# Optimization experiments

Measured on AMD Instinct MI355X. Metric: run time of the kernel, lower is better.

## Reference

```python
import jax, jax.numpy as jnp
import numpy as np

B, S, D_IN, D_OUT = 4, 2048, 1024, 1024


def setup_inputs() -> dict:
    key = jax.random.key(0)
    ks = jax.random.split(key, 7)
    s_in = 1.0 / np.sqrt(D_IN)
    return {
        "x": jax.random.normal(ks[0], (B, S, D_IN), dtype=jnp.float32),
        "Wq": jax.random.uniform(ks[1], (D_IN, D_OUT), jnp.float32, -s_in, s_in),
        "bq": jax.random.uniform(ks[2], (D_OUT,), jnp.float32, -s_in, s_in),
        "Wk": jax.random.uniform(ks[3], (D_IN, D_OUT), jnp.float32, -s_in, s_in),
        "bk": jax.random.uniform(ks[4], (D_OUT,), jnp.float32, -s_in, s_in),
        "Wv": jax.random.uniform(ks[5], (D_IN, D_OUT), jnp.float32, -s_in, s_in),
        "bv": jax.random.uniform(ks[6], (D_OUT,), jnp.float32, -s_in, s_in),
    }


def reference(x, Wq, bq, Wk, bk, Wv, bv):
    # q,k,v: [B, S, D_OUT]
    q = jnp.einsum("bsd,de->bse", x, Wq) + bq
    k = jnp.einsum("bsd,de->bse", x, Wk) + bk
    v = jnp.einsum("bsd,de->bse", x, Wv) + bv
    scale = 1.0 / jnp.sqrt(jnp.asarray(q.shape[-1], q.dtype))
    scores = jnp.einsum("bqe,bke->bqk", q, k) * scale  # [B, S, S]
    attn = jax.nn.softmax(scores, axis=-1)
    return jnp.einsum("bqk,bke->bqe", attn, v)
```

## Files before the change

### kernel.cpp

```cpp
#include <hip/hip_runtime.h>
#include <hip/hip_bf16.h>
#include <stdint.h>


#define Bsz 4
#define Ssz 2048
#define Dsz 1024

typedef __attribute__((ext_vector_type(8))) short short8;
typedef __attribute__((ext_vector_type(4))) float floatx4;
typedef const __attribute__((address_space(1))) void* gptr_t;
typedef __attribute__((address_space(3))) void* lptr_t;

__device__ __forceinline__ ushort f32_to_bf16(float f) {
    union { float f; uint32_t u; } c; c.f = f;
    uint32_t u = c.u;
    u += 0x7fffu + ((u >> 16) & 1u);
    return (ushort)(u >> 16);
}

__device__ __forceinline__ void glds16(const ushort* g, ushort* l) {
    __builtin_amdgcn_global_load_lds((gptr_t)g, (lptr_t)l, 16, 0, 0);
}

__device__ __forceinline__ void barrier_raw() {
    asm volatile("" ::: "memory");
    __builtin_amdgcn_s_barrier();
    asm volatile("" ::: "memory");
}

#define MFMA_QUAD(MB, NB)                                                              \
    _Pragma("unroll")                                                                  \
    for (int m_ = 0; m_ < 4; m_++) {                                                   \
        _Pragma("unroll")                                                              \
        for (int n_ = 0; n_ < 2; n_++) {                                               \
            acc[(MB) * 4 + m_][(NB) * 2 + n_] = __builtin_amdgcn_mfma_f32_16x16x32_bf16( \
                af[m_][0], bf[(NB) * 2 + n_][0], acc[(MB) * 4 + m_][(NB) * 2 + n_], 0, 0, 0); \
            acc[(MB) * 4 + m_][(NB) * 2 + n_] = __builtin_amdgcn_mfma_f32_16x16x32_bf16( \
                af[m_][1], bf[(NB) * 2 + n_][1], acc[(MB) * 4 + m_][(NB) * 2 + n_], 0, 0, 0); \
        }                                                                              \
    }

#define LOAD_A(half)                                                                   \
    _Pragma("unroll")                                                                  \
    for (int m_ = 0; m_ < 4; m_++) {                                                   \
        af[m_][0] = *(const short8*)(lA + aBase + ((half) * 4 + m_) * 1024 + c0);      \
        af[m_][1] = *(const short8*)(lA + aBase + ((half) * 4 + m_) * 1024 + c1);      \
    }

#define LOAD_B(pn)                                                                     \
    _Pragma("unroll")                                                                  \
    for (int n_ = 0; n_ < 2; n_++) {                                                   \
        bf[(pn) * 2 + n_][0] = *(const short8*)(lB + bBase + ((pn) * 2 + n_) * 1024 + c0); \
        bf[(pn) * 2 + n_][1] = *(const short8*)(lB + bBase + ((pn) * 2 + n_) * 1024 + c1); \
    }

template <int NT>
__device__ __forceinline__ void gemm256_core(
    const ushort* __restrict__ A, int lda,
    const ushort* __restrict__ Bt, int ldb,
    int row0, int col0, floatx4 (&acc)[8][4])
{
    __shared__ __align__(16) ushort lsA[2][256 * 64];
    __shared__ __align__(16) ushort lsB[2][256 * 64];

    const int tid  = threadIdx.x;
    const int lane = tid & 63;
    const int wave = tid >> 6;
    const int wr   = (wave >> 2) * 128;
    const int wc   = (wave & 3) * 64;
    const int m16  = lane & 15;
    const int quad = lane >> 4;

#pragma unroll
    for (int i = 0; i < 8; i++)
#pragma unroll
        for (int j = 0; j < 4; j++) acc[i][j] = (floatx4){0.f, 0.f, 0.f, 0.f};

    const int sRow = tid >> 3;
    const int sC   = ((tid & 7) ^ (sRow & 7)) * 8;
    const ushort* aSrc = A  + (size_t)(row0 + sRow) * lda + sC;
    const ushort* bSrc = Bt + (size_t)(col0 + sRow) * ldb + sC;
    ushort* dA = &lsA[0][0] + tid * 8;
    ushort* dB = &lsB[0][0] + tid * 8;

    const int aBase = (wr + m16) * 64;
    const int bBase = (wc + m16) * 64;
    const int c0 = (quad ^ (m16 & 7)) * 8;
    const int c1 = c0 ^ 32;

    auto stage = [&](int kt, int buf, int pair) {
        const size_t ko = (size_t)kt * 64;
        const int bo = buf * 16384;
        if (pair == 0) {
            glds16(aSrc + ko,                      dA + bo);
            glds16(aSrc + ko + (size_t)64 * lda,   dA + bo + 4096);
        } else if (pair == 1) {
            glds16(aSrc + ko + (size_t)128 * lda,  dA + bo + 8192);
            glds16(aSrc + ko + (size_t)192 * lda,  dA + bo + 12288);
        } else if (pair == 2) {
            glds16(bSrc + ko,                      dB + bo);
            glds16(bSrc + ko + (size_t)64 * ldb,   dB + bo + 4096);
        } else {
            glds16(bSrc + ko + (size_t)128 * ldb,  dB + bo + 8192);
            glds16(bSrc + ko + (size_t)192 * ldb,  dB + bo + 12288);
        }
    };

    stage(0, 0, 0); stage(0, 0, 1); stage(0, 0, 2); stage(0, 0, 3);
    stage(1, 1, 0);
    asm volatile("s_waitcnt vmcnt(2)" ::: "memory");
    barrier_raw();

    short8 af[4][2], bf[4][2];

    for (int kt = 0; kt < NT; ++kt) {
        const int buf = kt & 1;
        const ushort* lA = &lsA[buf][0];
        const ushort* lB = &lsB[buf][0];
        const bool pf1 = (kt + 1 < NT);

        LOAD_A(0);
        LOAD_B(0);
        if (pf1) stage(kt + 1, buf ^ 1, 1);
        barrier_raw();
        __builtin_amdgcn_s_setprio(1);
        MFMA_QUAD(0, 0);
        __builtin_amdgcn_s_setprio(0);
        barrier_raw();

        LOAD_B(1);
        if (pf1) stage(kt + 1, buf ^ 1, 2);
        barrier_raw();
        __builtin_amdgcn_s_setprio(1);
        MFMA_QUAD(0, 1);
        __builtin_amdgcn_s_setprio(0);
        barrier_raw();

        LOAD_A(1);
        if (pf1) stage(kt + 1, buf ^ 1, 3);
        barrier_raw();
        __builtin_amdgcn_s_setprio(1);
        MFMA_QUAD(1, 0);
        __builtin_amdgcn_s_setprio(0);
        barrier_raw();

        if (kt + 2 < NT) stage(kt + 2, buf, 0);
        __builtin_amdgcn_s_setprio(1);
        MFMA_QUAD(1, 1);
        __builtin_amdgcn_s_setprio(0);
        if (kt + 2 < NT)      { asm volatile("s_waitcnt vmcnt(2)" ::: "memory"); }
        else if (kt + 1 < NT) { asm volatile("s_waitcnt vmcnt(0)" ::: "memory"); }
        barrier_raw();
    }
}

__global__ __launch_bounds__(512, 2) void k_qkv256(
    const ushort* __restrict__ xb, const ushort* __restrict__ Wt,
    const float* __restrict__ bq, const float* __restrict__ bk,
    const float* __restrict__ bv, ushort* __restrict__ QKV,
    ushort* __restrict__ Vt)
{
    const int bid = blockIdx.x;
    const int wg  = (bid & 7) * 48 + (bid >> 3);
    const int bm  = wg & 31;
    const int bn  = wg >> 5;
    const int row0  = bm * 256;
    const int col0n = bn * 256;

    floatx4 acc[8][4];
    gemm256_core<16>(xb, Dsz, Wt, Dsz, row0, col0n, acc);

    const int tid  = threadIdx.x;
    const int lane = tid & 63;
    const int wave = tid >> 6;
    const int wr   = (wave >> 2) * 128;
    const int wc   = (wave & 3) * 64;
    const int m16  = lane & 15;
    const int quad = lane >> 4;

    const int z     = bn >> 2;
    const int colz0 = col0n & 1023;

    if (z == 0) {
#pragma unroll
        for (int ni = 0; ni < 4; ni++) {
            const int colz = colz0 + wc + ni * 16 + m16;
            const float bqv = bq[colz];
#pragma unroll
            for (int mi = 0; mi < 8; mi++) {
                const int grow0 = row0 + wr + mi * 16 + quad * 4;
#pragma unroll
                for (int j = 0; j < 4; j++)
                    QKV[(size_t)(grow0 + j) * Dsz + colz] =
                        f32_to_bf16((acc[mi][ni][j] + bqv) * 0.03125f);
            }
        }
    } else if (z == 1) {
        ushort* Kout = QKV + (size_t)(Bsz * Ssz) * Dsz;
#pragma unroll
        for (int ni = 0; ni < 4; ni++) {
            const int colz = colz0 + wc + ni * 16 + m16;
            const float bkv = bk[colz];
#pragma unroll
            for (int mi = 0; mi < 8; mi++) {
                const int grow0 = row0 + wr + mi * 16 + quad * 4;
#pragma unroll
                for (int j = 0; j < 4; j++)
                    Kout[(size_t)(grow0 + j) * Dsz + colz] =
                        f32_to_bf16(acc[mi][ni][j] + bkv);
            }
        }
    } else {
#pragma unroll
        for (int ni = 0; ni < 4; ni++) {
            const int colz = colz0 + wc + ni * 16 + m16;
            const float bvv = bv[colz];
#pragma unroll
            for (int mi = 0; mi < 8; mi++) {
                const int grow0 = row0 + wr + mi * 16 + quad * 4;
                ushort4 vpack;
                vpack.x = f32_to_bf16(acc[mi][ni][0] + bvv);
                vpack.y = f32_to_bf16(acc[mi][ni][1] + bvv);
                vpack.z = f32_to_bf16(acc[mi][ni][2] + bvv);
                vpack.w = f32_to_bf16(acc[mi][ni][3] + bvv);
                const int batch = grow0 >> 11;
                const int s0 = grow0 & (Ssz - 1);
                *(ushort4*)&Vt[(size_t)batch * Dsz * Ssz + (size_t)colz * Ssz + s0] = vpack;
            }
        }
    }
}

__global__ __launch_bounds__(512, 2) void k_scores256(
    const ushort* __restrict__ QKV, float* __restrict__ scores)
{
    const int bid = blockIdx.x;
    const int wg  = (bid & 7) * 32 + (bid >> 3);
    const int b   = wg >> 6;
    const int bm  = (wg >> 3) & 7;
    const int bn  = wg & 7;
    const int row0 = bm * 256;
    const int col0 = bn * 256;

    const ushort* Q  = QKV + (size_t)b * Ssz * Dsz;
    const ushort* Kb = QKV + (size_t)(Bsz + b) * Ssz * Dsz;

    floatx4 acc[8][4];
    gemm256_core<16>(Q, Dsz, Kb, Dsz, row0, col0, acc);

    const int tid  = threadIdx.x;
    const int lane = tid & 63;
    const int wave = tid >> 6;
    const int wr   = (wave >> 2) * 128;
    const int wc   = (wave & 3) * 64;
    const int m16  = lane & 15;
    const int quad = lane >> 4;

    float* out = scores + (size_t)b * Ssz * Ssz;
#pragma unroll
    for (int ni = 0; ni < 4; ni++) {
        const int gcol = col0 + wc + ni * 16 + m16;
#pragma unroll
        for (int mi = 0; mi < 8; mi++) {
            const int grow0 = row0 + wr + mi * 16 + quad * 4;
#pragma unroll
            for (int j = 0; j < 4; j++)
                out[(size_t)(grow0 + j) * Ssz + gcol] = acc[mi][ni][j];
        }
    }
}

template <bool OUT_BF16>
__device__ __forceinline__ void gemm128(
    int bx, int by,
    const ushort* __restrict__ A, int lda,
    const ushort* __restrict__ Bt, int ldb,
    int K,
    void* __restrict__ Cout, int ldc,
    const float* __restrict__ bias, float alpha)
{
    __shared__ ushort lsA[2][128 * 32];
    __shared__ ushort lsB[2][128 * 32];

    const int tid  = threadIdx.x;
    const int row0 = by * 128;
    const int col0 = bx * 128;

    const int lane = tid & 63;
    const int wave = tid >> 6;
    const int wr   = (wave >> 1) * 64;
    const int wc   = (wave & 1) * 64;
    const int m16  = lane & 15;
    const int quad = lane >> 4;

    floatx4 acc[4][4];
#pragma unroll
    for (int i = 0; i < 4; i++)
#pragma unroll
        for (int j = 0; j < 4; j++) acc[i][j] = (floatx4){0.f, 0.f, 0.f, 0.f};

    const int srow = tid >> 2;
    const int skc  = (tid & 3) ^ ((srow >> 1) & 3);
    const ushort* ga = A  + (size_t)(row0 + srow) * lda + skc * 8;
    const ushort* gb = Bt + (size_t)(col0 + srow) * ldb + skc * 8;
    const int aoff = (quad ^ ((m16 >> 1) & 3)) * 8;

    __builtin_amdgcn_global_load_lds((gptr_t)(ga),                     (lptr_t)(lsA[0] + tid * 8),        16, 0, 0);
    __builtin_amdgcn_global_load_lds((gptr_t)(ga + (size_t)64 * lda), (lptr_t)(lsA[0] + 2048 + tid * 8), 16, 0, 0);
    __builtin_amdgcn_global_load_lds((gptr_t)(gb),                     (lptr_t)(lsB[0] + tid * 8),        16, 0, 0);
    __builtin_amdgcn_global_load_lds((gptr_t)(gb + (size_t)64 * ldb), (lptr_t)(lsB[0] + 2048 + tid * 8), 16, 0, 0);

    for (int k0 = 0; k0 < K; k0 += 32) {
        const int cur = (k0 >> 5) & 1;
        __syncthreads();
        if (k0 + 32 < K) {
            const int nxt = cur ^ 1;
            const int kn = k0 + 32;
            __builtin_amdgcn_global_load_lds((gptr_t)(ga + kn),                     (lptr_t)(lsA[nxt] + tid * 8),        16, 0, 0);
            __builtin_amdgcn_global_load_lds((gptr_t)(ga + kn + (size_t)64 * lda), (lptr_t)(lsA[nxt] + 2048 + tid * 8), 16, 0, 0);
            __builtin_amdgcn_global_load_lds((gptr_t)(gb + kn),                     (lptr_t)(lsB[nxt] + tid * 8),        16, 0, 0);
            __builtin_amdgcn_global_load_lds((gptr_t)(gb + kn + (size_t)64 * ldb), (lptr_t)(lsB[nxt] + 2048 + tid * 8), 16, 0, 0);
        }

        short8 af[4], bfr[4];
#pragma unroll
        for (int mi = 0; mi < 4; mi++)
            af[mi] = *(const short8*)&lsA[cur][(wr + mi * 16 + m16) * 32 + aoff];
#pragma unroll
        for (int ni = 0; ni < 4; ni++)
            bfr[ni] = *(const short8*)&lsB[cur][(wc + ni * 16 + m16) * 32 + aoff];
#pragma unroll
        for (int mi = 0; mi < 4; mi++)
#pragma unroll
            for (int ni = 0; ni < 4; ni++)
                acc[mi][ni] = __builtin_amdgcn_mfma_f32_16x16x32_bf16(af[mi], bfr[ni], acc[mi][ni], 0, 0, 0);
    }

#pragma unroll
    for (int ni = 0; ni < 4; ni++) {
        const int gcol = col0 + wc + ni * 16 + m16;
        const float bv = bias ? bias[gcol] : 0.0f;
#pragma unroll
        for (int mi = 0; mi < 4; mi++) {
            const int grow0 = row0 + wr + mi * 16 + quad * 4;
#pragma unroll
            for (int j = 0; j < 4; j++) {
                float v = (acc[mi][ni][j] + bv) * alpha;
                if (OUT_BF16)
                    ((ushort*)Cout)[(size_t)(grow0 + j) * ldc + gcol] = f32_to_bf16(v);
                else
                    ((float*)Cout)[(size_t)(grow0 + j) * ldc + gcol] = v;
            }
        }
    }
}

__global__ __launch_bounds__(256) void k_cvt_x(const float* __restrict__ x, ushort* __restrict__ xb) {
    int i = (blockIdx.x * 256 + threadIdx.x) * 4;
    float4 v = *(const float4*)(x + i);
    ushort4 o;
    o.x = f32_to_bf16(v.x); o.y = f32_to_bf16(v.y);
    o.z = f32_to_bf16(v.z); o.w = f32_to_bf16(v.w);
    *(ushort4*)(xb + i) = o;
}

__global__ __launch_bounds__(256) void k_wt(const float* __restrict__ Wq, const float* __restrict__ Wk,
                                            const float* __restrict__ Wv, ushort* __restrict__ Wt) {
    __shared__ float tile[32][33];
    const int z = blockIdx.z;
    const float* W = (z == 0) ? Wq : ((z == 1) ? Wk : Wv);
    ushort* out = Wt + (size_t)z * Dsz * Dsz;
    const int kb = blockIdx.y * 32, nb = blockIdx.x * 32;
    const int tx = threadIdx.x, ty = threadIdx.y;
#pragma unroll
    for (int j = 0; j < 32; j += 8)
        tile[ty + j][tx] = W[(size_t)(kb + ty + j) * Dsz + nb + tx];
    __syncthreads();
#pragma unroll
    for (int j = 0; j < 32; j += 8)
        out[(size_t)(nb + ty + j) * Dsz + kb + tx] = f32_to_bf16(tile[tx][ty + j]);
}

__global__ __launch_bounds__(256) void k_softmax(float* __restrict__ scores) {
    const size_t row = blockIdx.x;
    float* rp = scores + row * Ssz;
    const int tid = threadIdx.x;
    float4 v0 = ((const float4*)rp)[tid];
    float4 v1 = ((const float4*)rp)[tid + 256];
    float m = fmaxf(fmaxf(fmaxf(v0.x, v0.y), fmaxf(v0.z, v0.w)),
                    fmaxf(fmaxf(v1.x, v1.y), fmaxf(v1.z, v1.w)));
#pragma unroll
    for (int o = 32; o > 0; o >>= 1) m = fmaxf(m, __shfl_down(m, o, 64));
    __shared__ float redm[4];
    if ((tid & 63) == 0) redm[tid >> 6] = m;
    __syncthreads();
    const float rm = fmaxf(fmaxf(redm[0], redm[1]), fmaxf(redm[2], redm[3]));
    v0.x = __expf(v0.x - rm); v0.y = __expf(v0.y - rm);
    v0.z = __expf(v0.z - rm); v0.w = __expf(v0.w - rm);
    v1.x = __expf(v1.x - rm); v1.y = __expf(v1.y - rm);
    v1.z = __expf(v1.z - rm); v1.w = __expf(v1.w - rm);
    float s = v0.x + v0.y + v0.z + v0.w + v1.x + v1.y + v1.z + v1.w;
#pragma unroll
    for (int o = 32; o > 0; o >>= 1) s += __shfl_down(s, o, 64);
    __shared__ float reds[4];
    if ((tid & 63) == 0) reds[tid >> 6] = s;
    __syncthreads();
    const float inv = 1.0f / (reds[0] + reds[1] + reds[2] + reds[3]);
    ushort4 o0, o1;
    o0.x = f32_to_bf16(v0.x * inv); o0.y = f32_to_bf16(v0.y * inv);
    o0.z = f32_to_bf16(v0.z * inv); o0.w = f32_to_bf16(v0.w * inv);
    o1.x = f32_to_bf16(v1.x * inv); o1.y = f32_to_bf16(v1.y * inv);
    o1.z = f32_to_bf16(v1.z * inv); o1.w = f32_to_bf16(v1.w * inv);
    ((ushort4*)rp)[tid] = o0;
    ((ushort4*)rp)[tid + 256] = o1;
}

__global__ __launch_bounds__(256) void k_pv(const float* __restrict__ scores, const ushort* __restrict__ Vt,
                                            float* __restrict__ out) {
    const int b = blockIdx.z;
    const int lin = blockIdx.y * 8 + blockIdx.x;
    const int c = lin & 7, m = lin >> 3;
    const int by = 2 * c + (m & 1);
    const int bx = m >> 1;
    const ushort* P = (const ushort*)(scores + (size_t)b * Ssz * Ssz);
    const ushort* Bt = Vt + (size_t)b * Dsz * Ssz;
    gemm128<false>(bx, by, P, 2 * Ssz, Bt, Ssz, Ssz, out + (size_t)b * Ssz * Dsz, Dsz, nullptr, 1.0f);
}

extern "C" void kernel_launch(void* const* d_in, const int* in_sizes, int n_in,
                              void* d_out, int out_size, void* d_ws, size_t ws_size,
                              hipStream_t stream) {
    const float* x  = (const float*)d_in[0];
    const float* Wq = (const float*)d_in[1];
    const float* bq = (const float*)d_in[2];
    const float* Wk = (const float*)d_in[3];
    const float* bk = (const float*)d_in[4];
    const float* Wv = (const float*)d_in[5];
    const float* bv = (const float*)d_in[6];
    float* out = (float*)d_out;

    char* ws = (char*)d_ws;
    ushort* xb     = (ushort*)(ws);
    ushort* Wt     = (ushort*)(ws + 16777216);
    ushort* QKV    = (ushort*)(ws + 23068672);
    ushort* Vt     = (ushort*)(ws + 73400320);
    float*  scores = (float*) (ws + 90177536);

    k_cvt_x<<<dim3(Bsz * Ssz * Dsz / (256 * 4)), dim3(256), 0, stream>>>(x, xb);
    k_wt<<<dim3(32, 32, 3), dim3(32, 8), 0, stream>>>(Wq, Wk, Wv, Wt);
    k_qkv256<<<dim3(384), dim3(512), 0, stream>>>(xb, Wt, bq, bk, bv, QKV, Vt);
    k_scores256<<<dim3(256), dim3(512), 0, stream>>>(QKV, scores);
    k_softmax<<<dim3(Bsz * Ssz), dim3(256), 0, stream>>>(scores);
    k_pv<<<dim3(Dsz / 128, Ssz / 128, Bsz), dim3(256), 0, stream>>>(scores, Vt, out);
}
```

Before: 291.5 us.

## Restructure GEMM core to 4-stage K=32 LDS pipeline with prefetch depth three

Replaces the double-buffered K=64 GEMM mainloop with a four-buffer K=32 pipeline that prefetches three tiles ahead. Each iteration has two MFMA phases instead of four, so there are fewer barriers per K-step, and the LDS swizzle changes to a 4-column XOR. The aim is to hide global-load latency better and cut synchronisation overhead. In exchange, the loop runs twice as many iterations, and the vmcnt accounting is more intricate and could be fragile. LDS footprint stays the same.

```diff
diff --git a/kernel.cpp b/kernel.cpp
--- a/kernel.cpp
+++ b/kernel.cpp
@@ -29,40 +29,33 @@
     asm volatile("" ::: "memory");
 }
 
-#define MFMA_QUAD(MB, NB)                                                              \
-    _Pragma("unroll")                                                                  \
-    for (int m_ = 0; m_ < 4; m_++) {                                                   \
-        _Pragma("unroll")                                                              \
-        for (int n_ = 0; n_ < 2; n_++) {                                               \
-            acc[(MB) * 4 + m_][(NB) * 2 + n_] = __builtin_amdgcn_mfma_f32_16x16x32_bf16( \
-                af[m_][0], bf[(NB) * 2 + n_][0], acc[(MB) * 4 + m_][(NB) * 2 + n_], 0, 0, 0); \
-            acc[(MB) * 4 + m_][(NB) * 2 + n_] = __builtin_amdgcn_mfma_f32_16x16x32_bf16( \
-                af[m_][1], bf[(NB) * 2 + n_][1], acc[(MB) * 4 + m_][(NB) * 2 + n_], 0, 0, 0); \
-        }                                                                              \
-    }
-
-#define LOAD_A(half)                                                                   \
-    _Pragma("unroll")                                                                  \
-    for (int m_ = 0; m_ < 4; m_++) {                                                   \
-        af[m_][0] = *(const short8*)(lA + aBase + ((half) * 4 + m_) * 1024 + c0);      \
-        af[m_][1] = *(const short8*)(lA + aBase + ((half) * 4 + m_) * 1024 + c1);      \
-    }
-
-#define LOAD_B(pn)                                                                     \
-    _Pragma("unroll")                                                                  \
-    for (int n_ = 0; n_ < 2; n_++) {                                                   \
-        bf[(pn) * 2 + n_][0] = *(const short8*)(lB + bBase + ((pn) * 2 + n_) * 1024 + c0); \
-        bf[(pn) * 2 + n_][1] = *(const short8*)(lB + bBase + ((pn) * 2 + n_) * 1024 + c1); \
+#define V2_LOAD_A(half)                                                        \
+    _Pragma("unroll")                                                          \
+    for (int m_ = 0; m_ < 4; m_++)                                             \
+        af[m_] = *(const short8*)(lA + aBase + (half) * 2048 + m_ * 512 + cA);
+
+#define V2_LOAD_B()                                                            \
+    _Pragma("unroll")                                                          \
+    for (int n_ = 0; n_ < 4; n_++)                                             \
+        bf[n_] = *(const short8*)(lB + bBase + n_ * 512 + cA);
+
+#define V2_MFMA(half)                                                          \
+    _Pragma("unroll")                                                          \
+    for (int m_ = 0; m_ < 4; m_++) {                                           \
+        _Pragma("unroll")                                                      \
+        for (int n_ = 0; n_ < 4; n_++)                                         \
+            acc[(half) * 4 + m_][n_] = __builtin_amdgcn_mfma_f32_16x16x32_bf16( \
+                af[m_], bf[n_], acc[(half) * 4 + m_][n_], 0, 0, 0);            \
     }
 
 template <int NT>
-__device__ __forceinline__ void gemm256_core(
+__device__ __forceinline__ void gemm256_v2(
     const ushort* __restrict__ A, int lda,
     const ushort* __restrict__ Bt, int ldb,
     int row0, int col0, floatx4 (&acc)[8][4])
 {
-    __shared__ __align__(16) ushort lsA[2][256 * 64];
-    __shared__ __align__(16) ushort lsB[2][256 * 64];
+    __shared__ __align__(16) ushort lsA[4][256 * 32];
+    __shared__ __align__(16) ushort lsB[4][256 * 32];
 
     const int tid  = threadIdx.x;
     const int lane = tid & 63;
@@ -77,80 +70,58 @@
 #pragma unroll
         for (int j = 0; j < 4; j++) acc[i][j] = (floatx4){0.f, 0.f, 0.f, 0.f};
 
-    const int sRow = tid >> 3;
-    const int sC   = ((tid & 7) ^ (sRow & 7)) * 8;
+    const int sRow = tid >> 2;
+    const int sC   = ((tid & 3) ^ (sRow & 3)) * 8;
     const ushort* aSrc = A  + (size_t)(row0 + sRow) * lda + sC;
     const ushort* bSrc = Bt + (size_t)(col0 + sRow) * ldb + sC;
-    ushort* dA = &lsA[0][0] + tid * 8;
-    ushort* dB = &lsB[0][0] + tid * 8;
-
-    const int aBase = (wr + m16) * 64;
-    const int bBase = (wc + m16) * 64;
-    const int c0 = (quad ^ (m16 & 7)) * 8;
-    const int c1 = c0 ^ 32;
-
-    auto stage = [&](int kt, int buf, int pair) {
-        const size_t ko = (size_t)kt * 64;
-        const int bo = buf * 16384;
-        if (pair == 0) {
-            glds16(aSrc + ko,                      dA + bo);
-            glds16(aSrc + ko + (size_t)64 * lda,   dA + bo + 4096);
-        } else if (pair == 1) {
-            glds16(aSrc + ko + (size_t)128 * lda,  dA + bo + 8192);
-            glds16(aSrc + ko + (size_t)192 * lda,  dA + bo + 12288);
-        } else if (pair == 2) {
-            glds16(bSrc + ko,                      dB + bo);
-            glds16(bSrc + ko + (size_t)64 * ldb,   dB + bo + 4096);
-        } else {
-            glds16(bSrc + ko + (size_t)128 * ldb,  dB + bo + 8192);
-            glds16(bSrc + ko + (size_t)192 * ldb,  dB + bo + 12288);
-        }
+
+    const int aBase = (wr + m16) * 32;
+    const int bBase = (wc + m16) * 32;
+    const int cA    = (quad ^ (m16 & 3)) * 8;
+
+    auto stageA = [&](int t) {
+        ushort* d = &lsA[t & 3][0] + tid * 8;
+        const ushort* s = aSrc + t * 32;
+        glds16(s, d);
+        glds16(s + (size_t)128 * lda, d + 4096);
     };
-
-    stage(0, 0, 0); stage(0, 0, 1); stage(0, 0, 2); stage(0, 0, 3);
-    stage(1, 1, 0);
-    asm volatile("s_waitcnt vmcnt(2)" ::: "memory");
+    auto stageB = [&](int t) {
+        ushort* d = &lsB[t & 3][0] + tid * 8;
+        const ushort* s = bSrc + t * 32;
+        glds16(s, d);
+        glds16(s + (size_t)128 * ldb, d + 4096);
+    };
+
+    stageA(0); stageB(0);
+    stageA(1); stageB(1);
+    stageA(2); stageB(2);
+    asm volatile("s_waitcnt vmcnt(8)" ::: "memory");
     barrier_raw();
 
-    short8 af[4][2], bf[4][2];
-
-    for (int kt = 0; kt < NT; ++kt) {
-        const int buf = kt & 1;
-        const ushort* lA = &lsA[buf][0];
-        const ushort* lB = &lsB[buf][0];
-        const bool pf1 = (kt + 1 < NT);
-
-        LOAD_A(0);
-        LOAD_B(0);
-        if (pf1) stage(kt + 1, buf ^ 1, 1);
+    short8 af[4], bf[4];
+
+    for (int t = 0; t < NT; ++t) {
+        const ushort* lA = &lsA[t & 3][0];
+        const ushort* lB = &lsB[t & 3][0];
+
+        V2_LOAD_B();
+        V2_LOAD_A(0);
+        if (t + 3 < NT) stageA(t + 3);
         barrier_raw();
         __builtin_amdgcn_s_setprio(1);
-        MFMA_QUAD(0, 0);
+        V2_MFMA(0);
         __builtin_amdgcn_s_setprio(0);
         barrier_raw();
 
-        LOAD_B(1);
-        if (pf1) stage(kt + 1, buf ^ 1, 2);
+        V2_LOAD_A(1);
+        if (t + 3 < NT) stageB(t + 3);
         barrier_raw();
         __builtin_amdgcn_s_setprio(1);
-        MFMA_QUAD(0, 1);
+        V2_MFMA(1);
         __builtin_amdgcn_s_setprio(0);
-        barrier_raw();
-
-        LOAD_A(1);
-        if (pf1) stage(kt + 1, buf ^ 1, 3);
-        barrier_raw();
-        __builtin_amdgcn_s_setprio(1);
-        MFMA_QUAD(1, 0);
-        __builtin_amdgcn_s_setprio(0);
-        barrier_raw();
-
-        if (kt + 2 < NT) stage(kt + 2, buf, 0);
-        __builtin_amdgcn_s_setprio(1);
-        MFMA_QUAD(1, 1);
-        __builtin_amdgcn_s_setprio(0);
-        if (kt + 2 < NT)      { asm volatile("s_waitcnt vmcnt(2)" ::: "memory"); }
-        else if (kt + 1 < NT) { asm volatile("s_waitcnt vmcnt(0)" ::: "memory"); }
+        if (t + 4 <= NT - 1)      { asm volatile("s_waitcnt vmcnt(8)" ::: "memory"); }
+        else if (t + 3 == NT - 1) { asm volatile("s_waitcnt vmcnt(4)" ::: "memory"); }
+        else if (t + 2 == NT - 1) { asm volatile("s_waitcnt vmcnt(0)" ::: "memory"); }
         barrier_raw();
     }
 }
@@ -169,7 +140,7 @@
     const int col0n = bn * 256;
 
     floatx4 acc[8][4];
-    gemm256_core<16>(xb, Dsz, Wt, Dsz, row0, col0n, acc);
+    gemm256_v2<32>(xb, Dsz, Wt, Dsz, row0, col0n, acc);
 
     const int tid  = threadIdx.x;
     const int lane = tid & 63;
@@ -247,7 +218,7 @@
     const ushort* Kb = QKV + (size_t)(Bsz + b) * Ssz * Dsz;
 
     floatx4 acc[8][4];
-    gemm256_core<16>(Q, Dsz, Kb, Dsz, row0, col0, acc);
+    gemm256_v2<32>(Q, Dsz, Kb, Dsz, row0, col0, acc);
 
     const int tid  = threadIdx.x;
     const int lane = tid & 63;
```

Measured after the change: 298.9 us. 2.5% more time.
